# Kernel optimization log

Hardware: AMD Instinct MI355X
Metric: run time of the kernel (lower is better)

The kernel has to match this reference:

```python
import jax, jax.numpy as jnp
import numpy as np

N = 50000      # nodes
E = 800000     # edges
INS = 128
H = 128
OUTS = 128
G = 512        # graphs in batch
BN_EPS = 1e-5


def _lin(k, fan_in, fan_out):
    s = 1.0 / np.sqrt(fan_in)
    kw, kb = jax.random.split(k)
    w = jax.random.uniform(kw, (fan_in, fan_out), minval=-s, maxval=s, dtype=jnp.float32)
    b = jax.random.uniform(kb, (fan_out,), minval=-s, maxval=s, dtype=jnp.float32)
    return w, b


def setup_inputs() -> dict:
    key = jax.random.key(0)
    ks = jax.random.split(key, 16)
    x = jax.random.normal(ks[0], (N, INS), dtype=jnp.float32)
    edge_src = jax.random.randint(ks[1], (E,), 0, N, dtype=jnp.int32)
    edge_dst = jax.random.randint(ks[2], (E,), 0, N, dtype=jnp.int32)
    ptr = jnp.sort(jax.random.randint(ks[3], (G + 1,), 0, N, dtype=jnp.int32))
    ptr = ptr.at[0].set(0).at[-1].set(N)
    w1a, b1a = _lin(ks[4], INS, H)
    w1b, b1b = _lin(ks[5], H, H)
    w2a, b2a = _lin(ks[6], H, H)
    w2b, b2b = _lin(ks[7], H, H)
    w3a, b3a = _lin(ks[8], H, H)
    w3b, b3b = _lin(ks[9], H, OUTS)
    g1 = jnp.ones((H,), jnp.float32); be1 = jnp.zeros((H,), jnp.float32)
    g2 = jnp.ones((H,), jnp.float32); be2 = jnp.zeros((H,), jnp.float32)
    g3 = jnp.ones((H,), jnp.float32); be3 = jnp.zeros((H,), jnp.float32)
    return dict(x=x, edge_src=edge_src, edge_dst=edge_dst, ptr=ptr,
                w1a=w1a, b1a=b1a, g1=g1, be1=be1, w1b=w1b, b1b=b1b,
                w2a=w2a, b2a=b2a, g2=g2, be2=be2, w2b=w2b, b2b=b2b,
                w3a=w3a, b3a=b3a, g3=g3, be3=be3, w3b=w3b, b3b=b3b)


def _bn(h, gamma, beta):
    # BatchNorm1d in training mode: stats over the node dimension
    mu = jnp.mean(h, axis=0)
    var = jnp.var(h, axis=0)
    return gamma * (h - mu) * jax.lax.rsqrt(var + BN_EPS) + beta


def _gin_layer(h, src, dst, wa, ba, gamma, beta, wb, bb):
    # GINConv (eps=0): mlp(x + sum_{j in N(i)} x_j)
    agg = jax.ops.segment_sum(h[src], dst, num_segments=N)  # [N, d]
    h = h + agg
    h = jax.nn.relu(_bn(h @ wa + ba, gamma, beta))
    h = jax.nn.relu(h @ wb + bb)
    return h


def reference(x, edge_src, edge_dst, ptr,
              w1a, b1a, g1, be1, w1b, b1b,
              w2a, b2a, g2, be2, w2b, b2b,
              w3a, b3a, g3, be3, w3b, b3b):
    h = _gin_layer(x, edge_src, edge_dst, w1a, b1a, g1, be1, w1b, b1b)
    h = _gin_layer(h, edge_src, edge_dst, w2a, b2a, g2, be2, w2b, b2b)
    h = _gin_layer(h, edge_src, edge_dst, w3a, b3a, g3, be3, w3b, b3b)
    # segment_csr(x, ptr, reduce='sum') readout
    seg = jnp.searchsorted(ptr, jnp.arange(N, dtype=jnp.int32), side='right') - 1
    return jax.ops.segment_sum(h, seg, num_segments=G)  # [G, OUTS]
```

## Files before the change

### kernel.cpp

```cpp
#include <hip/hip_runtime.h>

#define NNODES 50000
#define NEDGES 800000
#define HD 128
#define NG 512
#define BN_EPS 1e-5f
#define NTILE 3125
#define NSPLIT 8
#define NSB 49
#define AROW 136

typedef short bf16x8 __attribute__((ext_vector_type(8)));
typedef float floatx4 __attribute__((ext_vector_type(4)));

union U16 { uint4 u; bf16x8 h; };

__device__ __forceinline__ ushort f2bf(float f) {
    unsigned u = __float_as_uint(f);
    return (ushort)((u + 0x7fffu + ((u >> 16) & 1u)) >> 16);
}
__device__ __forceinline__ void unpack8(const uint4& u, float* f) {
    const unsigned* w = (const unsigned*)&u;
#pragma unroll
    for (int i = 0; i < 4; ++i) {
        f[2 * i]     = __uint_as_float(w[i] << 16);
        f[2 * i + 1] = __uint_as_float(w[i] & 0xffff0000u);
    }
}
__device__ __forceinline__ uint4 pack8(const float* f) {
    uint4 o;
    unsigned* w = (unsigned*)&o;
#pragma unroll
    for (int i = 0; i < 4; ++i)
        w[i] = (unsigned)f2bf(f[2 * i]) | ((unsigned)f2bf(f[2 * i + 1]) << 16);
    return o;
}


struct WP6 { const float* w[6]; };

__global__ __launch_bounds__(256, 4) void prep_kernel(
    const int* __restrict__ edst, int* __restrict__ cnt, int* __restrict__ rank,
    WP6 p, ushort* __restrict__ wf,
    const float* __restrict__ x, ushort* __restrict__ y) {
    __shared__ ushort wls[16384];
    __shared__ ushort abuf[16 * AROW];
    const int b = blockIdx.x, t = threadIdx.x;

    if (b < 3125) {
        int i = b * 256 + t;
        rank[i] = atomicAdd(&cnt[edst[i]], 1);
        return;
    }
    if (b < 3130) {
        int m = b - 3125 + 1;
        const float* W = p.w[m];
        ushort* o = wf + (size_t)m * 16384;
        for (int i = t; i < 16384; i += 256) {
            int j = i & 7, lane = (i >> 3) & 63, kc = (i >> 9) & 3, ct = i >> 11;
            int k = kc * 32 + (lane >> 4) * 8 + j;
            int n = ct * 16 + (lane & 15);
            o[i] = f2bf(W[k * HD + n]);
        }
        return;
    }

    const int row0 = (b - 3130) * 16;
    const int wave = t >> 6, lane = t & 63;
    const int quad = lane >> 4, l16 = lane & 15;

    {
        const float* W = p.w[0];
        uint4* s4 = (uint4*)wls;
#pragma unroll
        for (int i = 0; i < 8; ++i) {
            int f = i * 256 + t;
            int ln = f & 63;
            int kcct = f >> 6;
            int kc = kcct & 3, ct = kcct >> 2;
            int kbase = kc * 32 + (ln >> 4) * 8;
            int n = ct * 16 + (ln & 15);
            float fv[8];
#pragma unroll
            for (int j = 0; j < 8; ++j)
                fv[j] = W[(size_t)(kbase + j) * HD + n];
            s4[f] = pack8(fv);
        }
    }

    {
        int r = t >> 4, l = t & 15;
        const float* xp = x + (size_t)(row0 + r) * HD + l * 8;
        float4 v0 = ((const float4*)xp)[0];
        float4 v1 = ((const float4*)xp)[1];
        float f[8] = {v0.x, v0.y, v0.z, v0.w, v1.x, v1.y, v1.z, v1.w};
        *(uint4*)&abuf[r * AROW + l * 8] = pack8(f);
    }
    __syncthreads();

    U16 afr[4];
#pragma unroll
    for (int kc = 0; kc < 4; ++kc)
        afr[kc].u = *(const uint4*)&abuf[l16 * AROW + kc * 32 + quad * 8];

    const uint4* B4 = (const uint4*)wls;
    floatx4 zf = {0.f, 0.f, 0.f, 0.f};
    floatx4 acc[2] = {zf, zf};
#pragma unroll
    for (int kc = 0; kc < 4; ++kc)
#pragma unroll
        for (int c = 0; c < 2; ++c) {
            U16 bu; bu.u = B4[((2 * wave + c) * 4 + kc) * 64 + lane];
            acc[c] = __builtin_amdgcn_mfma_f32_16x16x32_bf16(afr[kc].h, bu.h, acc[c], 0, 0, 0);
        }
    __syncthreads();

    const int lrow = quad * 4;
#pragma unroll
    for (int c = 0; c < 2; ++c) {
        int col = (2 * wave + c) * 16 + l16;
#pragma unroll
        for (int reg = 0; reg < 4; ++reg)
            abuf[(lrow + reg) * AROW + col] = f2bf(acc[c][reg]);
    }
    __syncthreads();
    {
        uint4* o4 = (uint4*)y;
        int row = t >> 4, part = t & 15;
        o4[(size_t)(row0 + row) * 16 + part] = *(const uint4*)&abuf[row * AROW + part * 8];
    }
}


__global__ __launch_bounds__(1024) void scan_kernel(
    const int* __restrict__ cnt, int* __restrict__ bflag,
    int* __restrict__ rowp, int n) {
    __shared__ int s[1024];
    __shared__ int sprefix;
    const int t = threadIdx.x;
    const int bid = blockIdx.x;
    int i = bid * 1024 + t;
    int v = (i < n) ? cnt[i] : 0;
    s[t] = v;
    __syncthreads();
    for (int off = 1; off < 1024; off <<= 1) {
        int add = (t >= off) ? s[t - off] : 0;
        __syncthreads();
        s[t] += add;
        __syncthreads();
    }
    if (t == 0) {
        int pre = 0;
        if (bid > 0) {
            int f;
            do { f = atomicAdd(&bflag[bid - 1], 0); } while (f == 0);
            pre = f - 1;
        }
        atomicExch(&bflag[bid], pre + s[1023] + 1);
        sprefix = pre;
    }
    __syncthreads();
    if (i < n) rowp[i + 1] = s[t] + sprefix;
    if (i == 0) rowp[0] = 0;
}

__global__ void build_kernel(const int* __restrict__ src, const int* __restrict__ dst,
                             const int* __restrict__ rowp, const int* __restrict__ rank,
                             int* __restrict__ colv, int n) {
    int i = blockIdx.x * 256 + threadIdx.x;
    if (i < n) colv[rowp[dst[i]] + rank[i]] = src[i];
}


__global__ __launch_bounds__(256) void agg_kernel(
    const ushort* __restrict__ y, const int* __restrict__ rowp,
    const int* __restrict__ colv, const float* __restrict__ bias,
    ushort* __restrict__ z, float* __restrict__ ssum_p, float* __restrict__ ssq_p) {
    __shared__ float reds[4][HD];
    __shared__ float redq[4][HD];
    const int t = threadIdx.x;
    const int wave = t >> 6, lane = t & 63;
    const int node = blockIdx.x * 16 + (t >> 4);
    const int l = t & 15;
    const uint4* hp = (const uint4*)y;

    float a[8];
    unpack8(hp[(size_t)node * 16 + l], a);
    int beg = rowp[node], end = rowp[node + 1];
    int j = beg;
    for (; j + 3 < end; j += 4) {
        int c0 = colv[j], c1 = colv[j + 1], c2 = colv[j + 2], c3 = colv[j + 3];
        uint4 v0 = hp[(size_t)c0 * 16 + l];
        uint4 v1 = hp[(size_t)c1 * 16 + l];
        uint4 v2 = hp[(size_t)c2 * 16 + l];
        uint4 v3 = hp[(size_t)c3 * 16 + l];
        float b0[8], b1[8], b2[8], b3[8];
        unpack8(v0, b0); unpack8(v1, b1); unpack8(v2, b2); unpack8(v3, b3);
#pragma unroll
        for (int i = 0; i < 8; ++i) a[i] += (b0[i] + b1[i]) + (b2[i] + b3[i]);
    }
    for (; j < end; ++j) {
        float b[8];
        unpack8(hp[(size_t)colv[j] * 16 + l], b);
#pragma unroll
        for (int i = 0; i < 8; ++i) a[i] += b[i];
    }
    {
        float4 b0 = ((const float4*)(bias + l * 8))[0];
        float4 b1 = ((const float4*)(bias + l * 8))[1];
        a[0] += b0.x; a[1] += b0.y; a[2] += b0.z; a[3] += b0.w;
        a[4] += b1.x; a[5] += b1.y; a[6] += b1.z; a[7] += b1.w;
    }
    ((uint4*)z)[(size_t)node * 16 + l] = pack8(a);

    float s[8], q[8];
#pragma unroll
    for (int i = 0; i < 8; ++i) { s[i] = a[i]; q[i] = a[i] * a[i]; }
#pragma unroll
    for (int i = 0; i < 8; ++i) {
        s[i] += __shfl_xor(s[i], 16); s[i] += __shfl_xor(s[i], 32);
        q[i] += __shfl_xor(q[i], 16); q[i] += __shfl_xor(q[i], 32);
    }
    if (lane < 16) {
#pragma unroll
        for (int i = 0; i < 8; ++i) {
            reds[wave][lane * 8 + i] = s[i];
            redq[wave][lane * 8 + i] = q[i];
        }
    }
    __syncthreads();
    int slot = (blockIdx.x & (NSPLIT - 1)) * HD;
    if (t < HD) {
        atomicAdd(&ssum_p[slot + t], reds[0][t] + reds[1][t] + reds[2][t] + reds[3][t]);
    } else if (t < 2 * HD) {
        int c = t - HD;
        atomicAdd(&ssq_p[slot + c], redq[0][c] + redq[1][c] + redq[2][c] + redq[3][c]);
    }
}


__global__ __launch_bounds__(256, 3) void gemmBA_kernel(
    const ushort* __restrict__ z, const ushort* __restrict__ WfB,
    const ushort* __restrict__ WfA2, const float* __restrict__ biasB,
    ushort* __restrict__ yout,
    const float* __restrict__ gamma, const float* __restrict__ beta,
    const float* __restrict__ ssum_p, const float* __restrict__ ssq_p) {
    __shared__ ushort was[16384];
    __shared__ ushort cbuf[16 * AROW];
    __shared__ float sca[HD];
    __shared__ float shf[HD];
    const int t = threadIdx.x;
    const int wave = t >> 6, lane = t & 63;
    const int quad = lane >> 4, l16 = lane & 15;
    const int row0 = blockIdx.x * 16;
    const int rowA = row0 + l16;

    {
        const uint4* g = (const uint4*)WfA2;
        uint4 v[8];
#pragma unroll
        for (int i = 0; i < 8; ++i) v[i] = g[i * 256 + t];
        uint4* s = (uint4*)was;
#pragma unroll
        for (int i = 0; i < 8; ++i) s[i * 256 + t] = v[i];
    }

    const uint4* Wf4 = (const uint4*)WfB;
    uint4 bfr[2][4];
#pragma unroll
    for (int c = 0; c < 2; ++c)
#pragma unroll
        for (int kc = 0; kc < 4; ++kc)
            bfr[c][kc] = Wf4[((2 * wave + c) * 4 + kc) * 64 + lane];

    U16 afr[4];
    {
        const ushort* ap = z + (size_t)rowA * HD + quad * 8;
#pragma unroll
        for (int kc = 0; kc < 4; ++kc)
            afr[kc].u = *(const uint4*)(ap + kc * 32);
    }

    if (t < HD) {
        float s = 0.f, q = 0.f;
#pragma unroll
        for (int i = 0; i < NSPLIT; ++i) { s += ssum_p[i * HD + t]; q += ssq_p[i * HD + t]; }
        float mean = s / (float)NNODES;
        float var = q / (float)NNODES - mean * mean;
        float rstd = rsqrtf(var + BN_EPS);
        float sc = gamma[t] * rstd;
        sca[t] = sc;
        shf[t] = beta[t] - mean * sc;
    }
    __syncthreads();

#pragma unroll
    for (int kc = 0; kc < 4; ++kc) {
        float f[8];
        unpack8(afr[kc].u, f);
        int kb = kc * 32 + quad * 8;
        float4 s0 = ((const float4*)(sca + kb))[0];
        float4 s1 = ((const float4*)(sca + kb))[1];
        float4 h0 = ((const float4*)(shf + kb))[0];
        float4 h1 = ((const float4*)(shf + kb))[1];
        f[0] = fmaxf(fmaf(f[0], s0.x, h0.x), 0.f);
        f[1] = fmaxf(fmaf(f[1], s0.y, h0.y), 0.f);
        f[2] = fmaxf(fmaf(f[2], s0.z, h0.z), 0.f);
        f[3] = fmaxf(fmaf(f[3], s0.w, h0.w), 0.f);
        f[4] = fmaxf(fmaf(f[4], s1.x, h1.x), 0.f);
        f[5] = fmaxf(fmaf(f[5], s1.y, h1.y), 0.f);
        f[6] = fmaxf(fmaf(f[6], s1.z, h1.z), 0.f);
        f[7] = fmaxf(fmaf(f[7], s1.w, h1.w), 0.f);
        afr[kc].u = pack8(f);
    }

    floatx4 zf = {0.f, 0.f, 0.f, 0.f};
    floatx4 acc[2] = {zf, zf};
#pragma unroll
    for (int kc = 0; kc < 4; ++kc)
#pragma unroll
        for (int c = 0; c < 2; ++c) {
            U16 bu; bu.u = bfr[c][kc];
            acc[c] = __builtin_amdgcn_mfma_f32_16x16x32_bf16(afr[kc].h, bu.h, acc[c], 0, 0, 0);
        }

    const int lrow = quad * 4;
#pragma unroll
    for (int c = 0; c < 2; ++c) {
        int col = (2 * wave + c) * 16 + l16;
        float b = biasB[col];
#pragma unroll
        for (int reg = 0; reg < 4; ++reg)
            cbuf[(lrow + reg) * AROW + col] = f2bf(fmaxf(acc[c][reg] + b, 0.f));
    }
    __syncthreads();

    U16 a2[4];
#pragma unroll
    for (int kc = 0; kc < 4; ++kc)
        a2[kc].u = *(const uint4*)&cbuf[l16 * AROW + kc * 32 + quad * 8];
    const uint4* W2 = (const uint4*)was;
    floatx4 acc2[2] = {zf, zf};
#pragma unroll
    for (int kc = 0; kc < 4; ++kc)
#pragma unroll
        for (int c = 0; c < 2; ++c) {
            U16 bu; bu.u = W2[((2 * wave + c) * 4 + kc) * 64 + lane];
            acc2[c] = __builtin_amdgcn_mfma_f32_16x16x32_bf16(a2[kc].h, bu.h, acc2[c], 0, 0, 0);
        }
    __syncthreads();

#pragma unroll
    for (int c = 0; c < 2; ++c) {
        int col = (2 * wave + c) * 16 + l16;
#pragma unroll
        for (int reg = 0; reg < 4; ++reg)
            cbuf[(lrow + reg) * AROW + col] = f2bf(acc2[c][reg]);
    }
    __syncthreads();
    {
        uint4* o4 = (uint4*)yout;
        int row = t >> 4, part = t & 15;
        o4[(size_t)(row0 + row) * 16 + part] = *(const uint4*)&cbuf[row * AROW + part * 8];
    }
}


__global__ __launch_bounds__(256, 4) void gemmB2_kernel(
    const ushort* __restrict__ z, const ushort* __restrict__ WfB,
    const float* __restrict__ biasB,
    const float* __restrict__ gamma, const float* __restrict__ beta,
    const float* __restrict__ ssum_p, const float* __restrict__ ssq_p,
    const int* __restrict__ gptr, float* __restrict__ gout) {
    __shared__ float sca[HD];
    __shared__ float shf[HD];
    const int t = threadIdx.x;
    const int wave = t >> 6, lane = t & 63;
    const int quad = lane >> 4, l16 = lane & 15;
    const int row0 = blockIdx.x * 16;
    const int rowA = row0 + l16;

    const uint4* Wf4 = (const uint4*)WfB;
    uint4 bfr[2][4];
#pragma unroll
    for (int c = 0; c < 2; ++c)
#pragma unroll
        for (int kc = 0; kc < 4; ++kc)
            bfr[c][kc] = Wf4[((2 * wave + c) * 4 + kc) * 64 + lane];

    U16 afr[4];
    {
        const ushort* ap = z + (size_t)rowA * HD + quad * 8;
#pragma unroll
        for (int kc = 0; kc < 4; ++kc)
            afr[kc].u = *(const uint4*)(ap + kc * 32);
    }

    if (t < HD) {
        float s = 0.f, q = 0.f;
#pragma unroll
        for (int i = 0; i < NSPLIT; ++i) { s += ssum_p[i * HD + t]; q += ssq_p[i * HD + t]; }
        float mean = s / (float)NNODES;
        float var = q / (float)NNODES - mean * mean;
        float rstd = rsqrtf(var + BN_EPS);
        float sc = gamma[t] * rstd;
        sca[t] = sc;
        shf[t] = beta[t] - mean * sc;
    }
    __syncthreads();

#pragma unroll
    for (int kc = 0; kc < 4; ++kc) {
        float f[8];
        unpack8(afr[kc].u, f);
        int kb = kc * 32 + quad * 8;
        float4 s0 = ((const float4*)(sca + kb))[0];
        float4 s1 = ((const float4*)(sca + kb))[1];
        float4 h0 = ((const float4*)(shf + kb))[0];
        float4 h1 = ((const float4*)(shf + kb))[1];
        f[0] = fmaxf(fmaf(f[0], s0.x, h0.x), 0.f);
        f[1] = fmaxf(fmaf(f[1], s0.y, h0.y), 0.f);
        f[2] = fmaxf(fmaf(f[2], s0.z, h0.z), 0.f);
        f[3] = fmaxf(fmaf(f[3], s0.w, h0.w), 0.f);
        f[4] = fmaxf(fmaf(f[4], s1.x, h1.x), 0.f);
        f[5] = fmaxf(fmaf(f[5], s1.y, h1.y), 0.f);
        f[6] = fmaxf(fmaf(f[6], s1.z, h1.z), 0.f);
        f[7] = fmaxf(fmaf(f[7], s1.w, h1.w), 0.f);
        afr[kc].u = pack8(f);
    }

    floatx4 zf = {0.f, 0.f, 0.f, 0.f};
    floatx4 acc[2] = {zf, zf};
#pragma unroll
    for (int kc = 0; kc < 4; ++kc)
#pragma unroll
        for (int c = 0; c < 2; ++c) {
            U16 bu; bu.u = bfr[c][kc];
            acc[c] = __builtin_amdgcn_mfma_f32_16x16x32_bf16(afr[kc].h, bu.h, acc[c], 0, 0, 0);
        }

    int r_base = row0 + quad * 4;
    int lo = 0, hi = NG - 1;
    while (lo < hi) {
        int mid = (lo + hi) >> 1;
        if (r_base >= gptr[mid + 1]) lo = mid + 1; else hi = mid;
    }
    int segr[4];
    int sg = lo;
#pragma unroll
    for (int reg = 0; reg < 4; ++reg) {
        while (r_base + reg >= gptr[sg + 1]) ++sg;
        segr[reg] = sg;
    }
#pragma unroll
    for (int c = 0; c < 2; ++c) {
        int col = (2 * wave + c) * 16 + l16;
        float b = biasB[col];
        float run = 0.f;
        int cur = segr[0];
#pragma unroll
        for (int reg = 0; reg < 4; ++reg) {
            if (segr[reg] != cur) {
                if (run != 0.f) atomicAdd(&gout[cur * HD + col], run);
                run = 0.f;
                cur = segr[reg];
            }
            run += fmaxf(acc[c][reg] + b, 0.f);
        }
        if (run != 0.f) atomicAdd(&gout[cur * HD + col], run);
    }
}


extern "C" void kernel_launch(void* const* d_in, const int* in_sizes, int n_in,
                              void* d_out, int out_size, void* d_ws, size_t ws_size,
                              hipStream_t stream) {
    const float* x = (const float*)d_in[0];
    const int* esrc = (const int*)d_in[1];
    const int* edst = (const int*)d_in[2];
    const int* gptr = (const int*)d_in[3];
    const float* wA[3] = {(const float*)d_in[4], (const float*)d_in[10], (const float*)d_in[16]};
    const float* bA[3] = {(const float*)d_in[5], (const float*)d_in[11], (const float*)d_in[17]};
    const float* gm[3] = {(const float*)d_in[6], (const float*)d_in[12], (const float*)d_in[18]};
    const float* bt[3] = {(const float*)d_in[7], (const float*)d_in[13], (const float*)d_in[19]};
    const float* wB[3] = {(const float*)d_in[8], (const float*)d_in[14], (const float*)d_in[20]};
    const float* bB[3] = {(const float*)d_in[9], (const float*)d_in[15], (const float*)d_in[21]};

    char* w = (char*)d_ws;
    ushort* ybuf = (ushort*)w; w += (size_t)NNODES * HD * 2;
    ushort* zbuf = (ushort*)w; w += (size_t)NNODES * HD * 2;
    ushort* wf   = (ushort*)w; w += (size_t)6 * 16384 * 2;
    int* colv  = (int*)w;   w += (size_t)NEDGES * 4;
    int* rank  = (int*)w;   w += (size_t)NEDGES * 4;
    int* rowp  = (int*)w;   w += ((size_t)(NNODES + 1) * 4 + 15) & ~(size_t)15;
    char* zero_base = w;
    int* cnt   = (int*)w;   w += (size_t)NNODES * 4;
    int* bflag = (int*)w;   w += 64 * 4;
    float* ssum_p = (float*)w; w += 3 * NSPLIT * 128 * 4;
    float* ssq_p  = (float*)w; w += 3 * NSPLIT * 128 * 4;
    size_t zero_bytes = (size_t)(w - zero_base);

    hipMemsetAsync(zero_base, 0, zero_bytes, stream);
    hipMemsetAsync(d_out, 0, (size_t)NG * HD * 4, stream);

    WP6 wp;
    wp.w[0] = wA[0]; wp.w[1] = wB[0]; wp.w[2] = wA[1];
    wp.w[3] = wB[1]; wp.w[4] = wA[2]; wp.w[5] = wB[2];

    prep_kernel<<<6255, 256, 0, stream>>>(edst, cnt, rank, wp, wf, x, ybuf);
    scan_kernel<<<NSB, 1024, 0, stream>>>(cnt, bflag, rowp, NNODES);
    build_kernel<<<(NEDGES + 255) / 256, 256, 0, stream>>>(esrc, edst, rowp, rank, colv, NEDGES);

    for (int l = 0; l < 3; ++l) {
        agg_kernel<<<NTILE, 256, 0, stream>>>(
            ybuf, rowp, colv, bA[l], zbuf,
            ssum_p + l * NSPLIT * 128, ssq_p + l * NSPLIT * 128);
        if (l < 2) {
            gemmBA_kernel<<<NTILE, 256, 0, stream>>>(
                zbuf, wf + (size_t)(2 * l + 1) * 16384, wf + (size_t)(2 * l + 2) * 16384,
                bB[l], ybuf, gm[l], bt[l],
                ssum_p + l * NSPLIT * 128, ssq_p + l * NSPLIT * 128);
        } else {
            gemmB2_kernel<<<NTILE, 256, 0, stream>>>(
                zbuf, wf + (size_t)(2 * l + 1) * 16384, bB[l], gm[l], bt[l],
                ssum_p + l * NSPLIT * 128, ssq_p + l * NSPLIT * 128,
                gptr, (float*)d_out);
        }
    }
}
```

Baseline: 401.7 us.

## Deepen aggregation gather unroll, fold output memset into prep, raise gemm occupancy

The neighbour-gather loop in the aggregation kernel now issues eight independent row loads per iteration instead of four, with a four-edge remainder step, to keep more memory requests in flight. The separate output memset is removed and its zeroing moved into 64 extra blocks of the prep kernel, saving one launch. The gemmBA launch bound rises from 3 to 4 blocks per SM, which may limit registers and cause spills. The wider unroll also raises register pressure in the aggregation kernel.

```diff
diff --git a/kernel.cpp b/kernel.cpp
--- a/kernel.cpp
+++ b/kernel.cpp
@@ -42,7 +42,8 @@
 __global__ __launch_bounds__(256, 4) void prep_kernel(
     const int* __restrict__ edst, int* __restrict__ cnt, int* __restrict__ rank,
     WP6 p, ushort* __restrict__ wf,
-    const float* __restrict__ x, ushort* __restrict__ y) {
+    const float* __restrict__ x, ushort* __restrict__ y,
+    float4* __restrict__ gout4) {
     __shared__ ushort wls[16384];
     __shared__ ushort abuf[16 * AROW];
     const int b = blockIdx.x, t = threadIdx.x;
@@ -62,6 +63,10 @@
             int n = ct * 16 + (lane & 15);
             o[i] = f2bf(W[k * HD + n]);
         }
+        return;
+    }
+    if (b >= 6255) {
+        gout4[(b - 6255) * 256 + t] = make_float4(0.f, 0.f, 0.f, 0.f);
         return;
     }
 
@@ -188,16 +193,32 @@
     unpack8(hp[(size_t)node * 16 + l], a);
     int beg = rowp[node], end = rowp[node + 1];
     int j = beg;
-    for (; j + 3 < end; j += 4) {
-        int c0 = colv[j], c1 = colv[j + 1], c2 = colv[j + 2], c3 = colv[j + 3];
-        uint4 v0 = hp[(size_t)c0 * 16 + l];
-        uint4 v1 = hp[(size_t)c1 * 16 + l];
-        uint4 v2 = hp[(size_t)c2 * 16 + l];
-        uint4 v3 = hp[(size_t)c3 * 16 + l];
-        float b0[8], b1[8], b2[8], b3[8];
-        unpack8(v0, b0); unpack8(v1, b1); unpack8(v2, b2); unpack8(v3, b3);
-#pragma unroll
-        for (int i = 0; i < 8; ++i) a[i] += (b0[i] + b1[i]) + (b2[i] + b3[i]);
+    for (; j + 7 < end; j += 8) {
+        uint4 v[8];
+#pragma unroll
+        for (int e = 0; e < 8; ++e)
+            v[e] = hp[(size_t)colv[j + e] * 16 + l];
+#pragma unroll
+        for (int e = 0; e < 8; ++e) {
+            float b[8];
+            unpack8(v[e], b);
+#pragma unroll
+            for (int i = 0; i < 8; ++i) a[i] += b[i];
+        }
+    }
+    if (j + 3 < end) {
+        uint4 v[4];
+#pragma unroll
+        for (int e = 0; e < 4; ++e)
+            v[e] = hp[(size_t)colv[j + e] * 16 + l];
+#pragma unroll
+        for (int e = 0; e < 4; ++e) {
+            float b[8];
+            unpack8(v[e], b);
+#pragma unroll
+            for (int i = 0; i < 8; ++i) a[i] += b[i];
+        }
+        j += 4;
     }
     for (; j < end; ++j) {
         float b[8];
@@ -239,7 +260,7 @@
 }
 
 
-__global__ __launch_bounds__(256, 3) void gemmBA_kernel(
+__global__ __launch_bounds__(256, 4) void gemmBA_kernel(
     const ushort* __restrict__ z, const ushort* __restrict__ WfB,
     const ushort* __restrict__ WfA2, const float* __restrict__ biasB,
     ushort* __restrict__ yout,
@@ -501,13 +522,13 @@
     size_t zero_bytes = (size_t)(w - zero_base);
 
     hipMemsetAsync(zero_base, 0, zero_bytes, stream);
-    hipMemsetAsync(d_out, 0, (size_t)NG * HD * 4, stream);
 
     WP6 wp;
     wp.w[0] = wA[0]; wp.w[1] = wB[0]; wp.w[2] = wA[1];
     wp.w[3] = wB[1]; wp.w[4] = wA[2]; wp.w[5] = wB[2];
 
-    prep_kernel<<<6255, 256, 0, stream>>>(edst, cnt, rank, wp, wf, x, ybuf);
+    prep_kernel<<<6319, 256, 0, stream>>>(edst, cnt, rank, wp, wf, x, ybuf,
+                                          (float4*)d_out);
     scan_kernel<<<NSB, 1024, 0, stream>>>(cnt, bflag, rowp, NNODES);
     build_kernel<<<(NEDGES + 255) / 256, 256, 0, stream>>>(esrc, edst, rowp, rank, colv, NEDGES);
 
```

Result: no change. 403.6 us (+0.5%).
